# Performance work log

Hardware: AMD Instinct MI355X
Metric: run time of the kernel (lower is better)

## Reference

```python
import math
import jax, jax.numpy as jnp
import numpy as np

SEQ, BATCH, D_MODEL, HEADS = 2048, 2, 1024, 16
D_K = D_MODEL // HEADS


def setup_inputs() -> dict:
    key = jax.random.key(0)
    ks = jax.random.split(key, 11)
    s = 1.0 / math.sqrt(D_MODEL)
    inp = {
        "q": jax.random.normal(ks[0], (SEQ, BATCH, D_MODEL), jnp.float32),
        "k": jax.random.normal(ks[1], (SEQ, BATCH, D_MODEL), jnp.float32),
        "v": jax.random.normal(ks[2], (SEQ, BATCH, D_MODEL), jnp.float32),
        "Wq": jax.random.normal(ks[3], (D_MODEL, D_MODEL), jnp.float32) * s,
        "bq": jnp.zeros((D_MODEL,), jnp.float32),
        "Wk": jax.random.normal(ks[4], (D_MODEL, D_MODEL), jnp.float32) * s,
        "bk": jnp.zeros((D_MODEL,), jnp.float32),
        "Wv": jax.random.normal(ks[5], (D_MODEL, D_MODEL), jnp.float32) * s,
        "bv": jnp.zeros((D_MODEL,), jnp.float32),
        "Wo": jax.random.normal(ks[6], (D_MODEL, D_MODEL), jnp.float32) * s,
        "bo": jnp.zeros((D_MODEL,), jnp.float32),
    }
    return inp


def _proj(x, W, b):
    # [S,B,D] @ [D, H*Dk] -> [S,B,H,Dk]
    y = jnp.einsum('sbd,de->sbe', x, W) + b
    return y.reshape(x.shape[0], x.shape[1], HEADS, D_K)


def reference(q, k, v, Wq, bq, Wk, bk, Wv, bv, Wo, bo):
    scale = 1.0 / math.sqrt(D_K)
    query = _proj(q, Wq, bq)            # [i,b,h,d]
    key_ = _proj(k, Wk, bk)             # [j,b,h,d]
    value = _proj(v, Wv, bv)            # [j,b,h,d]
    scores = jnp.einsum('ibhd,jbhd->ijbh', query, key_) * scale
    attn = jax.nn.softmax(scores, axis=1)  # softmax over key axis j (dim=1)
    x = jnp.einsum('ijbh,jbhd->ibhd', attn, value)
    x = x.reshape(SEQ, BATCH, D_MODEL)
    return jnp.einsum('sbd,de->sbe', x, Wo) + bo
```

## Files before the change

### kernel.cpp

```cpp
#include <hip/hip_runtime.h>
#include <hip/hip_bf16.h>


typedef __attribute__((ext_vector_type(8))) short bf16x8;
typedef __attribute__((ext_vector_type(4))) float f32x4;

constexpr int SEQ   = 2048;
constexpr int BATCH = 2;
constexpr int DM    = 1024;
constexpr int DK    = 64;
constexpr int MR    = SEQ * BATCH;
constexpr int SST   = BATCH * DM;
constexpr int HD    = SEQ * DK;

__device__ __forceinline__ unsigned pkbf(float a, float b) {
    __hip_bfloat162 h = __float22bfloat162_rn(float2{a, b});
    union { __hip_bfloat162 h2; unsigned u; } cv;
    cv.h2 = h;
    return cv.u;
}

__device__ __forceinline__ f32x4 mfma16(bf16x8 a, bf16x8 b, f32x4 c) {
    return __builtin_amdgcn_mfma_f32_16x16x32_bf16(a, b, c, 0, 0, 0);
}

__device__ __forceinline__ void gl16(const unsigned short* g, unsigned short* l) {
    __builtin_amdgcn_global_load_lds(
        (const __attribute__((address_space(1))) void*)g,
        (__attribute__((address_space(3))) void*)l, 16, 0, 0);
}

__global__ __launch_bounds__(256)
void wt_prep_all(const float* __restrict__ w0, const float* __restrict__ w1,
                 const float* __restrict__ w2, const float* __restrict__ w3,
                 unsigned short* __restrict__ o0, unsigned short* __restrict__ o1,
                 unsigned short* __restrict__ o2, unsigned short* __restrict__ o3)
{
    const int z = blockIdx.z;
    const float* W = (z == 0) ? w0 : (z == 1) ? w1 : (z == 2) ? w2 : w3;
    unsigned short* Wt = (z == 0) ? o0 : (z == 1) ? o1 : (z == 2) ? o2 : o3;

    const int t = threadIdx.x;
    const int e = blockIdx.x * 64 + (t & 63);
    const int dq = blockIdx.y * 256 + (t >> 6) * 64;
    unsigned short* orow = Wt + (size_t)e * DM + dq;
#pragma unroll
    for (int c = 0; c < 8; ++c) {
        float f[8];
#pragma unroll
        for (int j = 0; j < 8; ++j)
            f[j] = W[(size_t)(dq + c * 8 + j) * DM + e];
        uint4 u = { pkbf(f[0], f[1]), pkbf(f[2], f[3]),
                    pkbf(f[4], f[5]), pkbf(f[6], f[7]) };
        *(uint4*)(orow + c * 8) = u;
    }
}

__global__ __launch_bounds__(256)
void gemm_qkv(const float* __restrict__ qa, const float* __restrict__ ka,
              const float* __restrict__ va,
              const unsigned short* __restrict__ wq, const unsigned short* __restrict__ wk,
              const unsigned short* __restrict__ wv,
              const float* __restrict__ bq, const float* __restrict__ bk,
              const float* __restrict__ bv,
              unsigned short* __restrict__ Qh, unsigned short* __restrict__ Kh,
              unsigned short* __restrict__ Vtp)
{
    constexpr int K = 1024;
    __shared__ short As[128][40];
    __shared__ unsigned short Bs[128 * 32];

    const int z = blockIdx.z;
    const float* A = (z == 0) ? qa : (z == 1) ? ka : va;
    const unsigned short* Bt = (z == 0) ? wq : (z == 1) ? wk : wv;
    const float* bias = (z == 0) ? bq : (z == 1) ? bk : bv;

    const int tid = threadIdx.x;
    const int bn = blockIdx.x, bm = blockIdx.y;
    const int wave = tid >> 6, lane = tid & 63;
    const int wr = wave >> 1, wc = wave & 1;
    const int lrow = lane & 15, g = lane >> 4;
    const int srow = tid >> 1, shalf = (tid & 1) * 16;
    const int gr = lane >> 2, gc = (lane & 3) * 8;

    f32x4 acc[4][4] = {};

    for (int k0 = 0; k0 < K; k0 += 32) {
        gl16(Bt + (size_t)(bn * 128 + wave * 32 + gr) * K + k0 + gc,
             Bs + (wave * 32) * 32);
        gl16(Bt + (size_t)(bn * 128 + wave * 32 + 16 + gr) * K + k0 + gc,
             Bs + (wave * 32 + 16) * 32);
        {
            const float* ap = A + (size_t)(bm * 128 + srow) * K + k0 + shalf;
            float4 f0 = ((const float4*)ap)[0];
            float4 f1 = ((const float4*)ap)[1];
            float4 f2 = ((const float4*)ap)[2];
            float4 f3 = ((const float4*)ap)[3];
            uint4 lo = { pkbf(f0.x, f0.y), pkbf(f0.z, f0.w),
                         pkbf(f1.x, f1.y), pkbf(f1.z, f1.w) };
            uint4 hi = { pkbf(f2.x, f2.y), pkbf(f2.z, f2.w),
                         pkbf(f3.x, f3.y), pkbf(f3.z, f3.w) };
            *(uint4*)&As[srow][shalf] = lo;
            *(uint4*)&As[srow][shalf + 8] = hi;
        }
        __syncthreads();

        bf16x8 af[4], bfr[4];
#pragma unroll
        for (int i = 0; i < 4; ++i)
            af[i] = *(const bf16x8*)&As[wr * 64 + i * 16 + lrow][g * 8];
#pragma unroll
        for (int j = 0; j < 4; ++j)
            bfr[j] = *(const bf16x8*)&Bs[(wc * 64 + j * 16 + lrow) * 32 + g * 8];
#pragma unroll
        for (int i = 0; i < 4; ++i)
#pragma unroll
            for (int j = 0; j < 4; ++j)
                acc[i][j] = mfma16(af[i], bfr[j], acc[i][j]);
        __syncthreads();
    }

#pragma unroll
    for (int j = 0; j < 4; ++j) {
        const int col = bn * 128 + wc * 64 + j * 16 + lrow;
        const float bb = bias[col];
        const int h = col >> 6, d = col & 63;
#pragma unroll
        for (int i = 0; i < 4; ++i) {
            const int row0 = bm * 128 + wr * 64 + i * 16 + 4 * g;
#pragma unroll
            for (int r = 0; r < 4; ++r) {
                const float v = acc[i][j][r] + bb;
                const unsigned short bfv = (unsigned short)(pkbf(v, v) & 0xffffu);
                const int row = row0 + r;
                const int s = row >> 1, b = row & 1;
                if (z != 2) {
                    unsigned short* C = (z == 0) ? Qh : Kh;
                    C[(size_t)(b * 16 + h) * HD + s * 64 + d] = bfv;
                } else {
                    const int st = s >> 6, sl = s & 63;
                    const int kc = sl >> 5, r5 = sl & 31;
                    const int h2 = r5 >> 4, gg = (r5 >> 2) & 3, jj = r5 & 3;
                    const int sp = kc * 32 + gg * 8 + h2 * 4 + jj;
                    Vtp[(size_t)(b * 16 + h) * HD + (size_t)d * SEQ + st * 64 + sp] = bfv;
                }
            }
        }
    }
}

__global__ __launch_bounds__(256)
void attn_mfma(const unsigned short* __restrict__ Qh,
               const unsigned short* __restrict__ Kh,
               const unsigned short* __restrict__ Vtp,
               unsigned short* __restrict__ Xp)
{
    __shared__ unsigned short lds[16384];

    const int tid = threadIdx.x;
    const int fid = blockIdx.x;
    const int xcd = fid & 7, idx = fid >> 3;
    const int bh = xcd * 4 + (idx >> 4);
    const int qt = idx & 15;

    const int wave = tid >> 6, lane = tid & 63;
    const int lrow = lane & 15, g = lane >> 4;
    const int s7 = lrow & 7;
    const int q0w = qt * 128 + wave * 32;
    const float CE = 0.18033688011112042592f;

    const unsigned short* qb = Qh + (size_t)bh * HD;
    const unsigned short* kb = Kh + (size_t)bh * HD;
    const unsigned short* vb = Vtp + (size_t)bh * HD;

    unsigned short* K0 = lds;
    unsigned short* V0 = lds + 4096;
    unsigned short* K1 = lds + 8192;
    unsigned short* V1 = lds + 12288;

    const int r8 = lane >> 3, c8 = lane & 7;
    const unsigned short* ksrcA = kb + (size_t)(wave * 16 + r8) * 64 + (c8 ^ r8) * 8;
    const unsigned short* ksrcB = ksrcA + 8 * 64;
    const unsigned short* vsrcA = vb + (size_t)(wave * 16 + r8) * SEQ + (c8 ^ r8) * 8;
    const unsigned short* vsrcB = vsrcA + 8 * SEQ;

    auto stage = [&](unsigned short* kbuf, unsigned short* vbuf, int t) {
        const size_t ko = (size_t)t * 4096;
        const size_t vo = (size_t)t * 64;
        gl16(ksrcA + ko, kbuf + wave * 1024);
        gl16(ksrcB + ko, kbuf + wave * 1024 + 512);
        gl16(vsrcA + vo, vbuf + wave * 1024);
        gl16(vsrcB + vo, vbuf + wave * 1024 + 512);
    };

    bf16x8 bq[2][2];
#pragma unroll
    for (int qi = 0; qi < 2; ++qi)
#pragma unroll
        for (int dc = 0; dc < 2; ++dc)
            bq[qi][dc] = *(const bf16x8*)(qb + (size_t)(q0w + qi * 16 + lrow) * 64
                                             + dc * 32 + g * 8);

    f32x4 oacc[4][2] = {};
    float lsum0 = 0.f, lsum1 = 0.f;

    const int off0 = lrow * 64 + ((g ^ s7) * 8);
    const int off1 = lrow * 64 + (((4 + g) ^ s7) * 8);

    auto compute = [&](const unsigned short* kbuf, const unsigned short* vbuf) {
        bf16x8 ak[4][2];
#pragma unroll
        for (int kt = 0; kt < 4; ++kt) {
            ak[kt][0] = *(const bf16x8*)(kbuf + kt * 1024 + off0);
            ak[kt][1] = *(const bf16x8*)(kbuf + kt * 1024 + off1);
        }

        uint4 pbu[2][2];
#pragma unroll
        for (int qi = 0; qi < 2; ++qi) {
            float ll = 0.f;
#pragma unroll
            for (int kt = 0; kt < 4; ++kt) {
                f32x4 s = { 0.f, 0.f, 0.f, 0.f };
                s = mfma16(ak[kt][0], bq[qi][0], s);
                s = mfma16(ak[kt][1], bq[qi][1], s);
                const float p0 = __builtin_amdgcn_exp2f(s[0] * CE);
                const float p1 = __builtin_amdgcn_exp2f(s[1] * CE);
                const float p2 = __builtin_amdgcn_exp2f(s[2] * CE);
                const float p3 = __builtin_amdgcn_exp2f(s[3] * CE);
                ll += (p0 + p1) + (p2 + p3);
                const unsigned lo = pkbf(p0, p1);
                const unsigned hi = pkbf(p2, p3);
                if (kt & 1) { pbu[kt >> 1][qi].z = lo; pbu[kt >> 1][qi].w = hi; }
                else        { pbu[kt >> 1][qi].x = lo; pbu[kt >> 1][qi].y = hi; }
            }
            if (qi == 0) lsum0 += ll; else lsum1 += ll;
        }

        bf16x8 av[4][2];
#pragma unroll
        for (int dt = 0; dt < 4; ++dt) {
            av[dt][0] = *(const bf16x8*)(vbuf + dt * 1024 + off0);
            av[dt][1] = *(const bf16x8*)(vbuf + dt * 1024 + off1);
        }

        __builtin_amdgcn_s_setprio(1);
#pragma unroll
        for (int kc = 0; kc < 2; ++kc)
#pragma unroll
            for (int dt = 0; dt < 4; ++dt)
#pragma unroll
                for (int qi = 0; qi < 2; ++qi) {
                    union { uint4 u; bf16x8 v; } cv;
                    cv.u = pbu[kc][qi];
                    oacc[dt][qi] = mfma16(av[dt][kc], cv.v, oacc[dt][qi]);
                }
        __builtin_amdgcn_s_setprio(0);
    };

    stage(K0, V0, 0);
    asm volatile("s_waitcnt vmcnt(0)" ::: "memory");
    __syncthreads();

#pragma unroll 1
    for (int tt = 0; tt < 16; ++tt) {
        stage(K1, V1, 2 * tt + 1);
        compute(K0, V0);
        __syncthreads();
        if (tt < 15) stage(K0, V0, 2 * tt + 2);
        compute(K1, V1);
        __syncthreads();
    }

    float l0 = lsum0; l0 += __shfl_xor(l0, 16); l0 += __shfl_xor(l0, 32);
    float l1 = lsum1; l1 += __shfl_xor(l1, 16); l1 += __shfl_xor(l1, 32);
    const float inv0 = 1.0f / l0, inv1 = 1.0f / l1;

    unsigned short (*osh)[72] = (unsigned short (*)[72])(lds + wave * 32 * 72);
#pragma unroll
    for (int qi = 0; qi < 2; ++qi) {
        const float inv = qi ? inv1 : inv0;
#pragma unroll
        for (int dt = 0; dt < 4; ++dt) {
            const int d0 = dt * 16 + 4 * g;
            const unsigned u0 = pkbf(oacc[dt][qi][0] * inv, oacc[dt][qi][1] * inv);
            const unsigned u1 = pkbf(oacc[dt][qi][2] * inv, oacc[dt][qi][3] * inv);
            *(unsigned*)&osh[qi * 16 + lrow][d0] = u0;
            *(unsigned*)&osh[qi * 16 + lrow][d0 + 2] = u1;
        }
    }
    const int ql = lane >> 1;
    const int dh = (lane & 1) * 32;
    unsigned short* xrow = Xp + (size_t)(q0w + ql) * SST + bh * 64 + dh;
#pragma unroll
    for (int c = 0; c < 4; ++c) {
        uint4 vv = *(const uint4*)&osh[ql][dh + c * 8];
        *(uint4*)(xrow + c * 8) = vv;
    }
}

__global__ __launch_bounds__(256)
void gemm_out(const unsigned short* __restrict__ Xp,
              const unsigned short* __restrict__ WtO,
              const float* __restrict__ bias, float* __restrict__ out)
{
    constexpr int K = 1024, N = 1024;
    __shared__ unsigned short As[128 * 32];
    __shared__ unsigned short Bs[64 * 32];

    const int tid = threadIdx.x;
    const int bn = blockIdx.x, bm = blockIdx.y;
    const int wave = tid >> 6, lane = tid & 63;
    const int wr = wave >> 1, wc = wave & 1;
    const int lrow = lane & 15, g = lane >> 4;
    const int gr = lane >> 2, gc = (lane & 3) * 8;

    f32x4 acc[4][2] = {};

    for (int k0 = 0; k0 < K; k0 += 32) {
        gl16(Xp + (size_t)(bm * 128 + wave * 32 + gr) * K + k0 + gc,
             As + (wave * 32) * 32);
        gl16(Xp + (size_t)(bm * 128 + wave * 32 + 16 + gr) * K + k0 + gc,
             As + (wave * 32 + 16) * 32);
        gl16(WtO + (size_t)(bn * 64 + wave * 16 + gr) * K + k0 + gc,
             Bs + (wave * 16) * 32);
        __syncthreads();

        bf16x8 af[4], bfr[2];
#pragma unroll
        for (int i = 0; i < 4; ++i)
            af[i] = *(const bf16x8*)&As[(wr * 64 + i * 16 + lrow) * 32 + g * 8];
#pragma unroll
        for (int j = 0; j < 2; ++j)
            bfr[j] = *(const bf16x8*)&Bs[(wc * 32 + j * 16 + lrow) * 32 + g * 8];
#pragma unroll
        for (int i = 0; i < 4; ++i)
#pragma unroll
            for (int j = 0; j < 2; ++j)
                acc[i][j] = mfma16(af[i], bfr[j], acc[i][j]);
        __syncthreads();
    }

#pragma unroll
    for (int j = 0; j < 2; ++j) {
        const int col = bn * 64 + wc * 32 + j * 16 + lrow;
        const float bb = bias[col];
#pragma unroll
        for (int i = 0; i < 4; ++i) {
            const int row0 = bm * 128 + wr * 64 + i * 16 + 4 * g;
#pragma unroll
            for (int r = 0; r < 4; ++r)
                out[(size_t)(row0 + r) * N + col] = acc[i][j][r] + bb;
        }
    }
}

extern "C" void kernel_launch(void* const* d_in, const int* in_sizes, int n_in,
                              void* d_out, int out_size, void* d_ws, size_t ws_size,
                              hipStream_t stream) {
    (void)in_sizes; (void)n_in; (void)out_size; (void)ws_size;

    const float* q  = (const float*)d_in[0];
    const float* k  = (const float*)d_in[1];
    const float* v  = (const float*)d_in[2];
    const float* Wq = (const float*)d_in[3];
    const float* bq = (const float*)d_in[4];
    const float* Wk = (const float*)d_in[5];
    const float* bk = (const float*)d_in[6];
    const float* Wv = (const float*)d_in[7];
    const float* bv = (const float*)d_in[8];
    const float* Wo = (const float*)d_in[9];
    const float* bo = (const float*)d_in[10];
    float* out = (float*)d_out;

    unsigned short* ws = (unsigned short*)d_ws;
    const size_t WSZ = (size_t)DM * DM;
    const size_t MSZ = (size_t)MR * DM;
    unsigned short* WtQ = ws;
    unsigned short* WtK = ws + WSZ;
    unsigned short* WtV = ws + 2 * WSZ;
    unsigned short* WtO = ws + 3 * WSZ;
    unsigned short* Qh  = ws + 4 * WSZ;
    unsigned short* Kh  = Qh + MSZ;
    unsigned short* Vtp = Kh + MSZ;
    unsigned short* Xp  = Vtp + MSZ;

    const dim3 blk(256);

    wt_prep_all<<<dim3(16, 4, 4), blk, 0, stream>>>(Wq, Wk, Wv, Wo, WtQ, WtK, WtV, WtO);

    gemm_qkv<<<dim3(8, 32, 3), blk, 0, stream>>>(q, k, v, WtQ, WtK, WtV,
                                                 bq, bk, bv, Qh, Kh, Vtp);

    attn_mfma<<<dim3(512), blk, 0, stream>>>(Qh, Kh, Vtp, Xp);

    gemm_out<<<dim3(16, 32), blk, 0, stream>>>(Xp, WtO, bo, out);
}
```

Baseline: 151.9 us.

## Use fragment-major LDS layout and XCD-aware block swizzle in projection GEMMs

The global-to-LDS load lane mapping changes so each 16-row tile is stored in the exact per-lane MFMA fragment order. Each lane then reads its bf16x8 fragment at lane*8, which should avoid LDS bank conflicts on the fragment reads. Both the QKV and output GEMMs also remap block indices so that blocks sharing the same A rows land on the same XCD, to improve L2 reuse. The cost is less coalesced global reads per row (16-byte chunks spread across 16 rows), and the remap assumes a fixed grid shape.

```diff
diff --git a/kernel.cpp b/kernel.cpp
--- a/kernel.cpp
+++ b/kernel.cpp
@@ -75,21 +75,25 @@
     const unsigned short* Bt = (z == 0) ? wq : (z == 1) ? wk : wv;
     const float* bias = (z == 0) ? bq : (z == 1) ? bk : bv;
 
+    const int l = blockIdx.x + 8 * blockIdx.y;
+    const int xcd = l & 7, jj0 = l >> 3;
+    const int bm = xcd * 4 + (jj0 >> 3);
+    const int bn = jj0 & 7;
+
     const int tid = threadIdx.x;
-    const int bn = blockIdx.x, bm = blockIdx.y;
     const int wave = tid >> 6, lane = tid & 63;
     const int wr = wave >> 1, wc = wave & 1;
     const int lrow = lane & 15, g = lane >> 4;
     const int srow = tid >> 1, shalf = (tid & 1) * 16;
-    const int gr = lane >> 2, gc = (lane & 3) * 8;
+    const int gr = lane & 15, gc = (lane >> 4) * 8;
 
     f32x4 acc[4][4] = {};
 
     for (int k0 = 0; k0 < K; k0 += 32) {
         gl16(Bt + (size_t)(bn * 128 + wave * 32 + gr) * K + k0 + gc,
-             Bs + (wave * 32) * 32);
+             Bs + (2 * wave) * 512);
         gl16(Bt + (size_t)(bn * 128 + wave * 32 + 16 + gr) * K + k0 + gc,
-             Bs + (wave * 32 + 16) * 32);
+             Bs + (2 * wave + 1) * 512);
         {
             const float* ap = A + (size_t)(bm * 128 + srow) * K + k0 + shalf;
             float4 f0 = ((const float4*)ap)[0];
@@ -111,7 +115,7 @@
             af[i] = *(const bf16x8*)&As[wr * 64 + i * 16 + lrow][g * 8];
 #pragma unroll
         for (int j = 0; j < 4; ++j)
-            bfr[j] = *(const bf16x8*)&Bs[(wc * 64 + j * 16 + lrow) * 32 + g * 8];
+            bfr[j] = *(const bf16x8*)&Bs[(wc * 4 + j) * 512 + lane * 8];
 #pragma unroll
         for (int i = 0; i < 4; ++i)
 #pragma unroll
@@ -140,8 +144,8 @@
                 } else {
                     const int st = s >> 6, sl = s & 63;
                     const int kc = sl >> 5, r5 = sl & 31;
-                    const int h2 = r5 >> 4, gg = (r5 >> 2) & 3, jj = r5 & 3;
-                    const int sp = kc * 32 + gg * 8 + h2 * 4 + jj;
+                    const int h2 = r5 >> 4, gg = (r5 >> 2) & 3, jv = r5 & 3;
+                    const int sp = kc * 32 + gg * 8 + h2 * 4 + jv;
                     Vtp[(size_t)(b * 16 + h) * HD + (size_t)d * SEQ + st * 64 + sp] = bfv;
                 }
             }
@@ -308,31 +312,35 @@
     __shared__ unsigned short As[128 * 32];
     __shared__ unsigned short Bs[64 * 32];
 
+    const int l = blockIdx.x + 16 * blockIdx.y;
+    const int xcd = l & 7, jj0 = l >> 3;
+    const int bm = xcd * 4 + (jj0 >> 4);
+    const int bn = jj0 & 15;
+
     const int tid = threadIdx.x;
-    const int bn = blockIdx.x, bm = blockIdx.y;
     const int wave = tid >> 6, lane = tid & 63;
     const int wr = wave >> 1, wc = wave & 1;
     const int lrow = lane & 15, g = lane >> 4;
-    const int gr = lane >> 2, gc = (lane & 3) * 8;
+    const int gr = lane & 15, gc = (lane >> 4) * 8;
 
     f32x4 acc[4][2] = {};
 
     for (int k0 = 0; k0 < K; k0 += 32) {
         gl16(Xp + (size_t)(bm * 128 + wave * 32 + gr) * K + k0 + gc,
-             As + (wave * 32) * 32);
+             As + (2 * wave) * 512);
         gl16(Xp + (size_t)(bm * 128 + wave * 32 + 16 + gr) * K + k0 + gc,
-             As + (wave * 32 + 16) * 32);
+             As + (2 * wave + 1) * 512);
         gl16(WtO + (size_t)(bn * 64 + wave * 16 + gr) * K + k0 + gc,
-             Bs + (wave * 16) * 32);
+             Bs + wave * 512);
         __syncthreads();
 
         bf16x8 af[4], bfr[2];
 #pragma unroll
         for (int i = 0; i < 4; ++i)
-            af[i] = *(const bf16x8*)&As[(wr * 64 + i * 16 + lrow) * 32 + g * 8];
+            af[i] = *(const bf16x8*)&As[(wr * 4 + i) * 512 + lane * 8];
 #pragma unroll
         for (int j = 0; j < 2; ++j)
-            bfr[j] = *(const bf16x8*)&Bs[(wc * 32 + j * 16 + lrow) * 32 + g * 8];
+            bfr[j] = *(const bf16x8*)&Bs[(wc * 2 + j) * 512 + lane * 8];
 #pragma unroll
         for (int i = 0; i < 4; ++i)
 #pragma unroll
```

Result: faster. 145.6 us (-4.2%).
